# Kernel optimization log

Hardware: AMD Instinct MI355X
Metric: run time of the kernel (lower is better)

Reference implementation:

```python
import jax, jax.numpy as jnp
import numpy as np
from jax import lax

DN = ('NCHW', 'OIHW', 'NCHW')
BN_EPS = 1e-5


def _conv(x, w, pad):
    # pad: list of (lo, hi) for H, W
    return lax.conv_general_dilated(x, w, (1, 1), pad, dimension_numbers=DN)


def _grid_sample_bilinear(img, grid):
    """F.grid_sample(img, grid, align_corners=True, padding_mode='zeros').
    img: [N,C,H,W], grid: [N,Ho,Wo,2] with (x,y) in [-1,1]."""
    N, C, H, W = img.shape
    gx, gy = grid[..., 0], grid[..., 1]
    # align_corners=True mapping to pixel coords
    ix = (gx + 1.0) * 0.5 * (W - 1)
    iy = (gy + 1.0) * 0.5 * (H - 1)
    x0 = jnp.floor(ix)
    y0 = jnp.floor(iy)
    x1 = x0 + 1.0
    y1 = y0 + 1.0
    # bilinear weights
    wa = (x1 - ix) * (y1 - iy)  # top-left (x0,y0)
    wb = (ix - x0) * (y1 - iy)  # top-right (x1,y0)
    wc = (x1 - ix) * (iy - y0)  # bottom-left (x0,y1)
    wd = (ix - x0) * (iy - y0)  # bottom-right (x1,y1)

    imgc = jnp.transpose(img, (0, 2, 3, 1))  # [N,H,W,C]
    b = jnp.arange(N)[:, None, None]

    def gather(xi, yi):
        valid = (xi >= 0) & (xi <= W - 1) & (yi >= 0) & (yi <= H - 1)
        xc = jnp.clip(xi, 0, W - 1).astype(jnp.int32)
        yc = jnp.clip(yi, 0, H - 1).astype(jnp.int32)
        v = imgc[b, yc, xc]  # [N,Ho,Wo,C]
        return v * valid[..., None].astype(img.dtype)

    out = (gather(x0, y0) * wa[..., None] + gather(x1, y0) * wb[..., None]
           + gather(x0, y1) * wc[..., None] + gather(x1, y1) * wd[..., None])
    return jnp.transpose(out, (0, 3, 1, 2))  # [N,C,Ho,Wo]


def setup_inputs() -> dict:
    key = jax.random.key(0)
    ks = jax.random.split(key, 12)
    N, C1, C2 = 8, 512, 256
    H, W = 64, 64
    x1 = jax.random.normal(ks[0], (N, C1, 2 * H, 2 * W), dtype=jnp.float32)
    x2 = jax.random.normal(ks[1], (N, C2, H, W), dtype=jnp.float32)
    w_change = jax.random.normal(ks[2], (C2, C1, 1, 1), dtype=jnp.float32) * 0.02
    b_change = jax.random.normal(ks[3], (C2,), dtype=jnp.float32) * 0.02
    w_cc1 = jax.random.normal(ks[4], (C2, 2 * C2, 1, 1), dtype=jnp.float32) * 0.02
    bn_gamma = 1.0 + 0.1 * jax.random.normal(ks[5], (C2,), dtype=jnp.float32)
    bn_beta = 0.1 * jax.random.normal(ks[6], (C2,), dtype=jnp.float32)
    bn_mean = 0.1 * jax.random.normal(ks[7], (C2,), dtype=jnp.float32)
    bn_var = jax.random.uniform(ks[8], (C2,), dtype=jnp.float32, minval=0.5, maxval=1.5)
    w_cc2 = jax.random.normal(ks[9], (4, C2, 3, 3), dtype=jnp.float32) * 0.02
    return {"x1": x1, "x2": x2, "w_change": w_change, "b_change": b_change,
            "w_cc1": w_cc1, "bn_gamma": bn_gamma, "bn_beta": bn_beta,
            "bn_mean": bn_mean, "bn_var": bn_var, "w_cc2": w_cc2}


def reference(x1, x2, w_change, b_change, w_cc1, bn_gamma, bn_beta, bn_mean, bn_var, w_cc2):
    # MaxPool2d(2,2)
    x1p = lax.reduce_window(x1, -jnp.inf, lax.max, (1, 1, 2, 2), (1, 1, 2, 2), 'VALID')
    # change: 1x1 conv with bias
    x1c = _conv(x1p, w_change, [(0, 0), (0, 0)]) + b_change[None, :, None, None]
    # concat + concat_conv (1x1 conv -> BN(eval) -> ReLU -> 3x3 conv)
    x = jnp.concatenate([x1c, x2], axis=1)
    x = _conv(x, w_cc1, [(0, 0), (0, 0)])
    inv = lax.rsqrt(bn_var + BN_EPS)
    x = (x - bn_mean[None, :, None, None]) * (inv * bn_gamma)[None, :, None, None] + bn_beta[None, :, None, None]
    x = jax.nn.relu(x)
    flow = _conv(x, w_cc2, [(1, 1), (1, 1)])  # [N,4,H,W]
    flow1 = flow[:, :2]
    flow2 = flow[:, 2:]

    N, _, H, W = x1c.shape
    # base grid: [...,0]=x over width, [...,1]=y over height
    xs = jnp.linspace(-1.0, 1.0, W, dtype=x1c.dtype)
    ys = jnp.linspace(-1.0, 1.0, H, dtype=x1c.dtype)
    base = jnp.stack(jnp.meshgrid(xs, ys, indexing='xy'), axis=-1)  # [H,W,2]
    norm = jnp.array([(W - 1) / 2.0, (H - 1) / 2.0], dtype=x1c.dtype)

    grid1 = base[None] + jnp.transpose(flow1, (0, 2, 3, 1)) / norm
    grid2 = base[None] + jnp.transpose(flow2, (0, 2, 3, 1)) / norm

    u1 = _grid_sample_bilinear(x1c, grid1)
    u2 = _grid_sample_bilinear(x2, grid2)
    return u1 + u2
```

## Files before the change

kernel.cpp:

```cpp
#include <hip/hip_runtime.h>
#include <hip/hip_bf16.h>

#define NB 8
#define C1 512
#define C2 256
#define HWSZ 4096
#define BN_EPS 1e-5f
#define P2 264

typedef __hip_bfloat16 bf16;
typedef __hip_bfloat162 bf162;
typedef __attribute__((ext_vector_type(8))) short short8v;
typedef __attribute__((ext_vector_type(4))) float f32x4;

static __device__ inline float us2f(unsigned short u) {
  union { unsigned u32; float f; } c; c.u32 = ((unsigned)u) << 16; return c.f;
}

static __device__ inline unsigned short f2bf(float f) {
  union { bf16 h; unsigned short u; } c;
  c.h = __float2bfloat16(f);
  return c.u;
}

static __device__ inline unsigned pack2(float a, float b) {
  union { unsigned u; bf162 h; } pk;
  pk.h = __float22bfloat162_rn(make_float2(a, b));
  return pk.u;
}

static __device__ inline uint2 pack4(float a, float b, float c, float d) {
  union { uint2 u; bf162 h[2]; } pk;
  pk.h[0] = __float22bfloat162_rn(make_float2(a, b));
  pk.h[1] = __float22bfloat162_rn(make_float2(c, d));
  return pk.u;
}

#define SWA(m_, c_)  (((((c_) >> 3) ^ (((m_) >> 3) & 3)) << 3) + ((c_) & 7))
#define SWA2(m_, c_) (((((c_) >> 3) ^ (((m_) >> 3) & 7)) << 3) + ((c_) & 7))

#define SBARQ() asm volatile("s_waitcnt lgkmcnt(0)\n\ts_barrier" ::: "memory")
#define SBAR()  asm volatile("s_barrier" ::: "memory")
#define LGKM0() asm volatile("s_waitcnt lgkmcnt(0)" ::: "memory")

__global__ __launch_bounds__(256) void k0_prep(
    const float* __restrict__ wch, const float* __restrict__ wcc1,
    const float* __restrict__ wcc2,
    unsigned short* __restrict__ wchB, unsigned short* __restrict__ wcc1B,
    float* __restrict__ wr, float* __restrict__ flow) {
  const int t = blockIdx.x * 256 + threadIdx.x;
  if (t < 262144) {
    const int which = t >> 17;
    const int r = t & 131071;
    const int i = r & 7;
    const int lane = (r >> 3) & 63;
    const int ntile = (r >> 9) & 15;
    const int kstep = r >> 13;
    const int ci = kstep * 32 + (lane >> 4) * 8 + i;
    const int co = ntile * 16 + (lane & 15);
    const float* s = which ? wcc1 : wch;
    unsigned short* d = which ? wcc1B : wchB;
    d[r] = f2bf(s[co * 512 + ci]);
  } else if (t < 262144 + 9216) {
    const int r = t - 262144;
    const int f = r / 2304;
    const int rr = r % 2304;
    const int ci = rr / 9;
    const int tt = rr % 9;
    wr[ci * 36 + (tt / 3) * 12 + (tt % 3) * 4 + f] = wcc2[r];
  } else if (t < 262144 + 9216 + 131072) {
    flow[t - 262144 - 9216] = 0.f;
  }
}

__global__ __launch_bounds__(512) void k12_fused(
    const float* __restrict__ x1, const float* __restrict__ x2,
    const unsigned short* __restrict__ wchB, const unsigned short* __restrict__ wcc1B,
    const float* __restrict__ bch,
    const float* __restrict__ gamma, const float* __restrict__ beta,
    const float* __restrict__ mean, const float* __restrict__ var,
    const float* __restrict__ wr,
    unsigned short* __restrict__ x1c_nhwc, unsigned short* __restrict__ x2_nhwc,
    float* __restrict__ flow) {
  __shared__ unsigned short As[64 * 40];
  __shared__ unsigned short As2[64 * P2];
  const int tid = threadIdx.x;
  const int lane = tid & 63;
  const int wv = tid >> 6;
  const int lrow = lane & 15;
  const int lgrp = lane >> 4;

  const int m0g = blockIdx.x * 64;
  const int n = m0g >> 12;
  const int hw0 = m0g & 4095;
  const int h = hw0 >> 6;

  f32x4 acc[4][2];
#pragma unroll
  for (int mt = 0; mt < 4; ++mt)
#pragma unroll
    for (int nt = 0; nt < 2; ++nt) acc[mt][nt] = (f32x4){0.f, 0.f, 0.f, 0.f};

  const int pmi = tid & 31;
  const int ms = pmi * 2;
  const int ch0 = (tid >> 5) * 2;

  const float* x1p = x1 + (size_t)n * C1 * 16384 + (size_t)(2 * h) * 128 + 2 * ms;

  float4 t0, b0, t1, b1;
#define LOADA(K0_) do { \
    const float* p_ = x1p + (size_t)((K0_) + ch0) * 16384; \
    t0 = *(const float4*)p_;            b0 = *(const float4*)(p_ + 128); \
    t1 = *(const float4*)(p_ + 16384);  b1 = *(const float4*)(p_ + 16384 + 128); \
  } while (0)
#define POOLA(U0_, U1_) do { \
    U0_ = pack2(fmaxf(fmaxf(t0.x, t0.y), fmaxf(b0.x, b0.y)), \
                fmaxf(fmaxf(t1.x, t1.y), fmaxf(b1.x, b1.y))); \
    U1_ = pack2(fmaxf(fmaxf(t0.z, t0.w), fmaxf(b0.z, b0.w)), \
                fmaxf(fmaxf(t1.z, t1.w), fmaxf(b1.z, b1.w))); \
  } while (0)

  unsigned uA0, uA1;
  LOADA(0);
  POOLA(uA0, uA1);
  LOADA(32);

  for (int ks = 0; ks < 16; ++ks) {
    SBARQ();
    *(unsigned*)&As[ms * 40 + SWA(ms, ch0)] = uA0;
    *(unsigned*)&As[(ms + 1) * 40 + SWA(ms + 1, ch0)] = uA1;
    LGKM0();
    SBAR();

    unsigned uN0, uN1;
    if (ks < 15) {
      POOLA(uN0, uN1);
      if (ks < 14) LOADA((ks + 2) * 32);
    }

    short8v a[4];
#pragma unroll
    for (int mt = 0; mt < 4; ++mt) {
      const int m = mt * 16 + lrow;
      a[mt] = *(const short8v*)&As[m * 40 + SWA(m, lgrp * 8)];
    }
#pragma unroll
    for (int nt = 0; nt < 2; ++nt) {
      const int ntile = wv * 2 + nt;
      const short8v b = *(const short8v*)&wchB[(size_t)((ks * 16 + ntile) * 64 + lane) * 8];
#pragma unroll
      for (int mt = 0; mt < 4; ++mt)
        acc[mt][nt] = __builtin_amdgcn_mfma_f32_16x16x32_bf16(a[mt], b, acc[mt][nt], 0, 0, 0);
    }
    if (ks < 15) { uA0 = uN0; uA1 = uN1; }
  }

  const int chB = tid >> 4;
  const int mqB = (tid & 15) * 4;
  float4 cf0 = *(const float4*)&x2[((size_t)(n * C2 + chB)) * HWSZ + hw0 + mqB];
  float4 cf1 = *(const float4*)&x2[((size_t)(n * C2 + 32 + chB)) * HWSZ + hw0 + mqB];

#pragma unroll
  for (int nt = 0; nt < 2; ++nt) {
    const int co = (wv * 2 + nt) * 16 + lrow;
    const float bias = bch[co];
#pragma unroll
    for (int mt = 0; mt < 4; ++mt) {
      const f32x4 v = acc[mt][nt];
      const uint2 pk = pack4(v.x + bias, v.y + bias, v.z + bias, v.w + bias);
      const int mb = mt * 16 + lgrp * 4;
      As2[(mb + 0) * P2 + SWA2(mb + 0, co)] = (unsigned short)(pk.x & 0xffffu);
      As2[(mb + 1) * P2 + SWA2(mb + 1, co)] = (unsigned short)(pk.x >> 16);
      As2[(mb + 2) * P2 + SWA2(mb + 2, co)] = (unsigned short)(pk.y & 0xffffu);
      As2[(mb + 3) * P2 + SWA2(mb + 3, co)] = (unsigned short)(pk.y >> 16);
      acc[mt][nt] = (f32x4){0.f, 0.f, 0.f, 0.f};
    }
  }
  LGKM0();
  SBAR();

  {
    const int mm = tid >> 3;
    const int cg = (tid & 7) * 32;
    const size_t ob = ((size_t)(m0g + mm)) * 256 + cg;
#pragma unroll
    for (int k = 0; k < 4; ++k) {
      const uint4 v = *(const uint4*)&As2[mm * P2 + SWA2(mm, cg + k * 8)];
      *(uint4*)&x1c_nhwc[ob + k * 8] = v;
    }
  }

#pragma unroll
  for (int ks = 0; ks < 8; ++ks) {
    short8v a[4];
#pragma unroll
    for (int mt = 0; mt < 4; ++mt) {
      const int m = mt * 16 + lrow;
      a[mt] = *(const short8v*)&As2[m * P2 + SWA2(m, ks * 32 + lgrp * 8)];
    }
#pragma unroll
    for (int nt = 0; nt < 2; ++nt) {
      const int ntile = wv * 2 + nt;
      const short8v b = *(const short8v*)&wcc1B[(size_t)((ks * 16 + ntile) * 64 + lane) * 8];
#pragma unroll
      for (int mt = 0; mt < 4; ++mt)
        acc[mt][nt] = __builtin_amdgcn_mfma_f32_16x16x32_bf16(a[mt], b, acc[mt][nt], 0, 0, 0);
    }
  }

  for (int ks = 8; ks < 16; ++ks) {
    const unsigned p0 = pack2(cf0.x, cf0.y);
    const unsigned p1 = pack2(cf0.z, cf0.w);
    cf0 = cf1;
    if (ks < 14) {
      cf1 = *(const float4*)&x2[((size_t)(n * C2 + (ks - 6) * 32 + chB)) * HWSZ + hw0 + mqB];
    }
    SBARQ();
    As[(mqB + 0) * 40 + SWA(mqB + 0, chB)] = (unsigned short)(p0 & 0xffffu);
    As[(mqB + 1) * 40 + SWA(mqB + 1, chB)] = (unsigned short)(p0 >> 16);
    As[(mqB + 2) * 40 + SWA(mqB + 2, chB)] = (unsigned short)(p1 & 0xffffu);
    As[(mqB + 3) * 40 + SWA(mqB + 3, chB)] = (unsigned short)(p1 >> 16);
    LGKM0();
    SBAR();

    {
      const int m = tid >> 3;
      const int c4 = (tid & 7) * 4;
      const uint2 v = *(const uint2*)&As[m * 40 + SWA(m, c4)];
      *(uint2*)&x2_nhwc[((size_t)(m0g + m)) * 256 + (ks - 8) * 32 + c4] = v;
    }

    short8v a[4];
#pragma unroll
    for (int mt = 0; mt < 4; ++mt) {
      const int m = mt * 16 + lrow;
      a[mt] = *(const short8v*)&As[m * 40 + SWA(m, lgrp * 8)];
    }
#pragma unroll
    for (int nt = 0; nt < 2; ++nt) {
      const int ntile = wv * 2 + nt;
      const short8v b = *(const short8v*)&wcc1B[(size_t)((ks * 16 + ntile) * 64 + lane) * 8];
#pragma unroll
      for (int mt = 0; mt < 4; ++mt)
        acc[mt][nt] = __builtin_amdgcn_mfma_f32_16x16x32_bf16(a[mt], b, acc[mt][nt], 0, 0, 0);
    }
  }

  SBARQ();
#pragma unroll
  for (int nt = 0; nt < 2; ++nt) {
    const int co = (wv * 2 + nt) * 16 + lrow;
    const float sc = gamma[co] * rsqrtf(var[co] + BN_EPS);
    const float sh = beta[co] - mean[co] * sc;
#pragma unroll
    for (int mt = 0; mt < 4; ++mt) {
      const f32x4 vv = acc[mt][nt];
      const uint2 pk = pack4(fmaxf(vv.x * sc + sh, 0.f), fmaxf(vv.y * sc + sh, 0.f),
                             fmaxf(vv.z * sc + sh, 0.f), fmaxf(vv.w * sc + sh, 0.f));
      const int mb = mt * 16 + lgrp * 4;
      As2[(mb + 0) * P2 + SWA2(mb + 0, co)] = (unsigned short)(pk.x & 0xffffu);
      As2[(mb + 1) * P2 + SWA2(mb + 1, co)] = (unsigned short)(pk.x >> 16);
      As2[(mb + 2) * P2 + SWA2(mb + 2, co)] = (unsigned short)(pk.y & 0xffffu);
      As2[(mb + 3) * P2 + SWA2(mb + 3, co)] = (unsigned short)(pk.y >> 16);
    }
  }
  LGKM0();
  SBAR();

  {
    const int xp = tid & 63;
    const int fh = tid >> 6;
    const int f = fh & 3;
    const int half = fh >> 2;
    float pm = 0.f, pz = 0.f, pp = 0.f;
    for (int ci = half * 128; ci < half * 128 + 128; ci += 2) {
      const float* w0 = wr + ci * 36 + f;
#pragma unroll
      for (int dx = 0; dx < 3; ++dx) {
        const int xs = xp + dx - 1;
        if ((unsigned)xs >= 64u) continue;
        const unsigned vv = *(const unsigned*)&As2[xs * P2 + SWA2(xs, ci)];
        const float v0 = us2f((unsigned short)(vv & 0xffffu));
        const float v1 = us2f((unsigned short)(vv >> 16));
        const float* wa = w0 + dx * 4;
        const float* wb = wa + 36;
        pm = fmaf(v0, wa[24], fmaf(v1, wb[24], pm));
        pz = fmaf(v0, wa[12], fmaf(v1, wb[12], pz));
        pp = fmaf(v0, wa[0],  fmaf(v1, wb[0],  pp));
      }
    }
    float* fb = flow + ((size_t)(n * 4 + f)) * HWSZ + xp;
    if (h >= 1)  atomicAdd(fb + (h - 1) * 64, pm);
    atomicAdd(fb + h * 64, pz);
    if (h <= 62) atomicAdd(fb + (h + 1) * 64, pp);
  }
#undef LOADA
#undef POOLA
}

__global__ __launch_bounds__(1024) void k4_sample(
    const float* __restrict__ flow,
    const unsigned short* __restrict__ x1c_nhwc,
    const unsigned short* __restrict__ x2_nhwc,
    float* __restrict__ out) {
  __shared__ float outT[256][65];
  __shared__ float flr[4][64];
  __shared__ int   toff[8][64];
  __shared__ float twt[8][64];

  const int tid = threadIdx.x;
  const int n = blockIdx.x >> 6;
  const int h = blockIdx.x & 63;
  const int wl = tid & 63;
  const int q = tid >> 6;

  if (tid < 256) {
    flr[tid >> 6][tid & 63] =
        flow[((size_t)(n * 4 + (tid >> 6))) * HWSZ + h * 64 + (tid & 63)];
  }
  __syncthreads();

  if (tid < 64) {
    const float fxv[2] = {flr[0][tid], flr[2][tid]};
    const float fyv[2] = {flr[1][tid], flr[3][tid]};
#pragma unroll
    for (int s = 0; s < 2; ++s) {
      const float ix = (float)tid + fxv[s], iy = (float)h + fyv[s];
      const float x0f = floorf(ix), y0f = floorf(iy);
      const float fx = ix - x0f, fy = iy - y0f;
      const int x0 = (int)x0f, y0 = (int)y0f, x1i = x0 + 1, y1i = y0 + 1;
      const float vx0 = (x0 >= 0 && x0 < 64) ? 1.f : 0.f;
      const float vx1 = (x1i >= 0 && x1i < 64) ? 1.f : 0.f;
      const float vy0 = (y0 >= 0 && y0 < 64) ? 1.f : 0.f;
      const float vy1 = (y1i >= 0 && y1i < 64) ? 1.f : 0.f;
      const int cx0 = min(max(x0, 0), 63), cx1 = min(max(x1i, 0), 63);
      const int cy0 = min(max(y0, 0), 63), cy1 = min(max(y1i, 0), 63);
      toff[s * 4 + 0][tid] = cy0 * 64 + cx0;
      toff[s * 4 + 1][tid] = cy0 * 64 + cx1;
      toff[s * 4 + 2][tid] = cy1 * 64 + cx0;
      toff[s * 4 + 3][tid] = cy1 * 64 + cx1;
      twt[s * 4 + 0][tid] = (1.f - fx) * (1.f - fy) * vx0 * vy0;
      twt[s * 4 + 1][tid] = fx * (1.f - fy) * vx1 * vy0;
      twt[s * 4 + 2][tid] = (1.f - fx) * fy * vx0 * vy1;
      twt[s * 4 + 3][tid] = fx * fy * vx1 * vy1;
    }
  }
  __syncthreads();

  {
    const unsigned short* pb1 = x1c_nhwc + (size_t)n * HWSZ * 256 + wl * 4;
    const unsigned short* pb2 = x2_nhwc + (size_t)n * HWSZ * 256 + wl * 4;
#pragma unroll
    for (int pp = 0; pp < 4; ++pp) {
      const int p = q * 4 + pp;
      float u0 = 0.f, u1 = 0.f, u2 = 0.f, u3 = 0.f;
#pragma unroll
      for (int t = 0; t < 8; ++t) {
        const int off = toff[t][p];
        const float wt = twt[t][p];
        const unsigned short* rp = (t < 4 ? pb1 : pb2) + (size_t)off * 256;
        const uint2 v = *(const uint2*)rp;
        u0 = fmaf(wt, us2f((unsigned short)(v.x & 0xffffu)), u0);
        u1 = fmaf(wt, us2f((unsigned short)(v.x >> 16)), u1);
        u2 = fmaf(wt, us2f((unsigned short)(v.y & 0xffffu)), u2);
        u3 = fmaf(wt, us2f((unsigned short)(v.y >> 16)), u3);
      }
      outT[wl * 4 + 0][p] = u0;
      outT[wl * 4 + 1][p] = u1;
      outT[wl * 4 + 2][p] = u2;
      outT[wl * 4 + 3][p] = u3;
    }
  }
  __syncthreads();

  {
    const int p = tid & 63;
    const int cg = (tid >> 6) * 16;
    const size_t ob = ((size_t)(n * C2 + cg)) * HWSZ + h * 64 + p;
#pragma unroll
    for (int j = 0; j < 16; ++j) {
      out[ob + (size_t)j * HWSZ] = outT[cg + j][p];
    }
  }
}

extern "C" void kernel_launch(void* const* d_in, const int* in_sizes, int n_in,
                              void* d_out, int out_size, void* d_ws, size_t ws_size,
                              hipStream_t stream) {
  const float* x1      = (const float*)d_in[0];
  const float* x2      = (const float*)d_in[1];
  const float* w_change= (const float*)d_in[2];
  const float* b_change= (const float*)d_in[3];
  const float* w_cc1   = (const float*)d_in[4];
  const float* bn_gamma= (const float*)d_in[5];
  const float* bn_beta = (const float*)d_in[6];
  const float* bn_mean = (const float*)d_in[7];
  const float* bn_var  = (const float*)d_in[8];
  const float* w_cc2   = (const float*)d_in[9];
  float* out = (float*)d_out;

  unsigned short* x1c_nhwc = (unsigned short*)d_ws;
  unsigned short* x2_nhwc  = (unsigned short*)((char*)d_ws + (16u << 20));
  float*          flow     = (float*)((char*)d_ws + (32u << 20));
  unsigned short* wchB     = (unsigned short*)((char*)d_ws + (32u << 20) + (512u << 10));
  unsigned short* wcc1B    = (unsigned short*)((char*)d_ws + (32u << 20) + (768u << 10));
  float*          wr       = (float*)((char*)d_ws + (33u << 20));

  k0_prep<<<1572, 256, 0, stream>>>(w_change, w_cc1, w_cc2, wchB, wcc1B, wr, flow);
  k12_fused<<<512, 512, 0, stream>>>(x1, x2, wchB, wcc1B, b_change,
                                     bn_gamma, bn_beta, bn_mean, bn_var, wr,
                                     x1c_nhwc, x2_nhwc, flow);
  k4_sample<<<512, 1024, 0, stream>>>(flow, x1c_nhwc, x2_nhwc, out);
}
```

Baseline: 140.0 us.

## Double fused GEMM block to 1024 threads, one N-tile per wave

The fused pool+1x1conv+concat-conv kernel now launches 1024 threads per block instead of 512. Each of the 16 waves owns a single 16-wide output-channel tile rather than two. Pooling loads, x2 staging, NHWC stores and the 3x3 flow reduction are all re-split across twice as many threads, each doing half the work. This is meant to raise wave-level parallelism and latency hiding per block, at the cost of more barrier participants, narrower per-thread memory accesses, and duplicated A-fragment LDS reads across more waves.

```diff
diff --git a/kernel.cpp b/kernel.cpp
--- a/kernel.cpp
+++ b/kernel.cpp
@@ -21,12 +21,6 @@
   union { bf16 h; unsigned short u; } c;
   c.h = __float2bfloat16(f);
   return c.u;
-}
-
-static __device__ inline unsigned pack2(float a, float b) {
-  union { unsigned u; bf162 h; } pk;
-  pk.h = __float22bfloat162_rn(make_float2(a, b));
-  return pk.u;
 }
 
 static __device__ inline uint2 pack4(float a, float b, float c, float d) {
@@ -73,7 +67,7 @@
   }
 }
 
-__global__ __launch_bounds__(512) void k12_fused(
+__global__ __launch_bounds__(1024) void k12_fused(
     const float* __restrict__ x1, const float* __restrict__ x2,
     const unsigned short* __restrict__ wchB, const unsigned short* __restrict__ wcc1B,
     const float* __restrict__ bch,
@@ -95,47 +89,43 @@
   const int hw0 = m0g & 4095;
   const int h = hw0 >> 6;
 
-  f32x4 acc[4][2];
-#pragma unroll
-  for (int mt = 0; mt < 4; ++mt)
-#pragma unroll
-    for (int nt = 0; nt < 2; ++nt) acc[mt][nt] = (f32x4){0.f, 0.f, 0.f, 0.f};
+  f32x4 acc[4];
+#pragma unroll
+  for (int mt = 0; mt < 4; ++mt) acc[mt] = (f32x4){0.f, 0.f, 0.f, 0.f};
 
   const int pmi = tid & 31;
   const int ms = pmi * 2;
-  const int ch0 = (tid >> 5) * 2;
+  const int chA = tid >> 5;
 
   const float* x1p = x1 + (size_t)n * C1 * 16384 + (size_t)(2 * h) * 128 + 2 * ms;
 
-  float4 t0, b0, t1, b1;
+  float4 t0, b0;
 #define LOADA(K0_) do { \
-    const float* p_ = x1p + (size_t)((K0_) + ch0) * 16384; \
-    t0 = *(const float4*)p_;            b0 = *(const float4*)(p_ + 128); \
-    t1 = *(const float4*)(p_ + 16384);  b1 = *(const float4*)(p_ + 16384 + 128); \
+    const float* p_ = x1p + (size_t)((K0_) + chA) * 16384; \
+    t0 = *(const float4*)p_;  b0 = *(const float4*)(p_ + 128); \
   } while (0)
 #define POOLA(U0_, U1_) do { \
-    U0_ = pack2(fmaxf(fmaxf(t0.x, t0.y), fmaxf(b0.x, b0.y)), \
-                fmaxf(fmaxf(t1.x, t1.y), fmaxf(b1.x, b1.y))); \
-    U1_ = pack2(fmaxf(fmaxf(t0.z, t0.w), fmaxf(b0.z, b0.w)), \
-                fmaxf(fmaxf(t1.z, t1.w), fmaxf(b1.z, b1.w))); \
+    U0_ = f2bf(fmaxf(fmaxf(t0.x, t0.y), fmaxf(b0.x, b0.y))); \
+    U1_ = f2bf(fmaxf(fmaxf(t0.z, t0.w), fmaxf(b0.z, b0.w))); \
   } while (0)
 
-  unsigned uA0, uA1;
+  unsigned short uA0, uA1;
   LOADA(0);
   POOLA(uA0, uA1);
   LOADA(32);
 
   for (int ks = 0; ks < 16; ++ks) {
     SBARQ();
-    *(unsigned*)&As[ms * 40 + SWA(ms, ch0)] = uA0;
-    *(unsigned*)&As[(ms + 1) * 40 + SWA(ms + 1, ch0)] = uA1;
+    As[ms * 40 + SWA(ms, chA)] = uA0;
+    As[(ms + 1) * 40 + SWA(ms + 1, chA)] = uA1;
     LGKM0();
     SBAR();
 
-    unsigned uN0, uN1;
     if (ks < 15) {
+      unsigned short uN0, uN1;
       POOLA(uN0, uN1);
       if (ks < 14) LOADA((ks + 2) * 32);
+      uA0 = uN0; uA1 = uN1;
     }
 
     short8v a[4];
@@ -144,47 +134,41 @@
       const int m = mt * 16 + lrow;
       a[mt] = *(const short8v*)&As[m * 40 + SWA(m, lgrp * 8)];
     }
-#pragma unroll
-    for (int nt = 0; nt < 2; ++nt) {
-      const int ntile = wv * 2 + nt;
-      const short8v b = *(const short8v*)&wchB[(size_t)((ks * 16 + ntile) * 64 + lane) * 8];
-#pragma unroll
-      for (int mt = 0; mt < 4; ++mt)
-        acc[mt][nt] = __builtin_amdgcn_mfma_f32_16x16x32_bf16(a[mt], b, acc[mt][nt], 0, 0, 0);
-    }
-    if (ks < 15) { uA0 = uN0; uA1 = uN1; }
-  }
-
-  const int chB = tid >> 4;
-  const int mqB = (tid & 15) * 4;
-  float4 cf0 = *(const float4*)&x2[((size_t)(n * C2 + chB)) * HWSZ + hw0 + mqB];
-  float4 cf1 = *(const float4*)&x2[((size_t)(n * C2 + 32 + chB)) * HWSZ + hw0 + mqB];
-
-#pragma unroll
-  for (int nt = 0; nt < 2; ++nt) {
-    const int co = (wv * 2 + nt) * 16 + lrow;
+    const short8v b = *(const short8v*)&wchB[(size_t)((ks * 16 + wv) * 64 + lane) * 8];
+#pragma unroll
+    for (int mt = 0; mt < 4; ++mt)
+      acc[mt] = __builtin_amdgcn_mfma_f32_16x16x32_bf16(a[mt], b, acc[mt], 0, 0, 0);
+  }
+
+  const int chB = tid >> 5;
+  const int mqB = (tid & 31) * 2;
+  float2 cf0 = *(const float2*)&x2[((size_t)(n * C2 + chB)) * HWSZ + hw0 + mqB];
+  float2 cf1 = *(const float2*)&x2[((size_t)(n * C2 + 32 + chB)) * HWSZ + hw0 + mqB];
+
+  {
+    const int co = wv * 16 + lrow;
     const float bias = bch[co];
 #pragma unroll
     for (int mt = 0; mt < 4; ++mt) {
-      const f32x4 v = acc[mt][nt];
+      const f32x4 v = acc[mt];
       const uint2 pk = pack4(v.x + bias, v.y + bias, v.z + bias, v.w + bias);
       const int mb = mt * 16 + lgrp * 4;
       As2[(mb + 0) * P2 + SWA2(mb + 0, co)] = (unsigned short)(pk.x & 0xffffu);
       As2[(mb + 1) * P2 + SWA2(mb + 1, co)] = (unsigned short)(pk.x >> 16);
       As2[(mb + 2) * P2 + SWA2(mb + 2, co)] = (unsigned short)(pk.y & 0xffffu);
       As2[(mb + 3) * P2 + SWA2(mb + 3, co)] = (unsigned short)(pk.y >> 16);
-      acc[mt][nt] = (f32x4){0.f, 0.f, 0.f, 0.f};
+      acc[mt] = (f32x4){0.f, 0.f, 0.f, 0.f};
     }
   }
   LGKM0();
   SBAR();
 
   {
-    const int mm = tid >> 3;
-    const int cg = (tid & 7) * 32;
+    const int mm = tid >> 4;
+    const int cg = (tid & 15) * 16;
     const size_t ob = ((size_t)(m0g + mm)) * 256 + cg;
 #pragma unroll
-    for (int k = 0; k < 4; ++k) {
+    for (int k = 0; k < 2; ++k) {
       const uint4 v = *(const uint4*)&As2[mm * P2 + SWA2(mm, cg + k * 8)];
       *(uint4*)&x1c_nhwc[ob + k * 8] = v;
     }
@@ -198,36 +182,30 @@
       const int m = mt * 16 + lrow;
       a[mt] = *(const short8v*)&As2[m * P2 + SWA2(m, ks * 32 + lgrp * 8)];
     }
-#pragma unroll
-    for (int nt = 0; nt < 2; ++nt) {
-      const int ntile = wv * 2 + nt;
-      const short8v b = *(const short8v*)&wcc1B[(size_t)((ks * 16 + ntile) * 64 + lane) * 8];
-#pragma unroll
-      for (int mt = 0; mt < 4; ++mt)
-        acc[mt][nt] = __builtin_amdgcn_mfma_f32_16x16x32_bf16(a[mt], b, acc[mt][nt], 0, 0, 0);
-    }
+    const short8v b = *(const short8v*)&wcc1B[(size_t)((ks * 16 + wv) * 64 + lane) * 8];
+#pragma unroll
+    for (int mt = 0; mt < 4; ++mt)
+      acc[mt] = __builtin_amdgcn_mfma_f32_16x16x32_bf16(a[mt], b, acc[mt], 0, 0, 0);
   }
 
   for (int ks = 8; ks < 16; ++ks) {
-    const unsigned p0 = pack2(cf0.x, cf0.y);
-    const unsigned p1 = pack2(cf0.z, cf0.w);
+    const unsigned short p0 = f2bf(cf0.x);
+    const unsigned short p1 = f2bf(cf0.y);
     cf0 = cf1;
     if (ks < 14) {
-      cf1 = *(const float4*)&x2[((size_t)(n * C2 + (ks - 6) * 32 + chB)) * HWSZ + hw0 + mqB];
+      cf1 = *(const float2*)&x2[((size_t)(n * C2 + (ks - 6) * 32 + chB)) * HWSZ + hw0 + mqB];
     }
     SBARQ();
-    As[(mqB + 0) * 40 + SWA(mqB + 0, chB)] = (unsigned short)(p0 & 0xffffu);
-    As[(mqB + 1) * 40 + SWA(mqB + 1, chB)] = (unsigned short)(p0 >> 16);
-    As[(mqB + 2) * 40 + SWA(mqB + 2, chB)] = (unsigned short)(p1 & 0xffffu);
-    As[(mqB + 3) * 40 + SWA(mqB + 3, chB)] = (unsigned short)(p1 >> 16);
+    As[(mqB + 0) * 40 + SWA(mqB + 0, chB)] = p0;
+    As[(mqB + 1) * 40 + SWA(mqB + 1, chB)] = p1;
     LGKM0();
     SBAR();
 
     {
-      const int m = tid >> 3;
-      const int c4 = (tid & 7) * 4;
-      const uint2 v = *(const uint2*)&As[m * 40 + SWA(m, c4)];
-      *(uint2*)&x2_nhwc[((size_t)(m0g + m)) * 256 + (ks - 8) * 32 + c4] = v;
+      const int m = tid >> 4;
+      const int c2 = (tid & 15) * 2;
+      const unsigned v = *(const unsigned*)&As[m * 40 + SWA(m, c2)];
+      *(unsigned*)&x2_nhwc[((size_t)(m0g + m)) * 256 + (ks - 8) * 32 + c2] = v;
     }
 
     short8v a[4];
@@ -236,25 +214,20 @@
       const int m = mt * 16 + lrow;
       a[mt] = *(const short8v*)&As[m * 40 + SWA(m, lgrp * 8)];
     }
-#pragma unroll
-    for (int nt = 0; nt < 2; ++nt) {
-      const int ntile = wv * 2 + nt;
-      const short8v b = *(const short8v*)&wcc1B[(size_t)((ks * 16 + ntile) * 64 + lane) * 8];
-#pragma unroll
-      for (int mt = 0; mt < 4; ++mt)
-        acc[mt][nt] = __builtin_amdgcn_mfma_f32_16x16x32_bf16(a[mt], b, acc[mt][nt], 0, 0, 0);
-    }
+    const short8v b = *(const short8v*)&wcc1B[(size_t)((ks * 16 + wv) * 64 + lane) * 8];
+#pragma unroll
+    for (int mt = 0; mt < 4; ++mt)
+      acc[mt] = __builtin_amdgcn_mfma_f32_16x16x32_bf16(a[mt], b, acc[mt], 0, 0, 0);
   }
 
   SBARQ();
-#pragma unroll
-  for (int nt = 0; nt < 2; ++nt) {
-    const int co = (wv * 2 + nt) * 16 + lrow;
+  {
+    const int co = wv * 16 + lrow;
     const float sc = gamma[co] * rsqrtf(var[co] + BN_EPS);
     const float sh = beta[co] - mean[co] * sc;
 #pragma unroll
     for (int mt = 0; mt < 4; ++mt) {
-      const f32x4 vv = acc[mt][nt];
+      const f32x4 vv = acc[mt];
       const uint2 pk = pack4(fmaxf(vv.x * sc + sh, 0.f), fmaxf(vv.y * sc + sh, 0.f),
                              fmaxf(vv.z * sc + sh, 0.f), fmaxf(vv.w * sc + sh, 0.f));
       const int mb = mt * 16 + lgrp * 4;
@@ -271,9 +244,9 @@
     const int xp = tid & 63;
     const int fh = tid >> 6;
     const int f = fh & 3;
-    const int half = fh >> 2;
+    const int quarter = fh >> 2;
     float pm = 0.f, pz = 0.f, pp = 0.f;
-    for (int ci = half * 128; ci < half * 128 + 128; ci += 2) {
+    for (int ci = quarter * 64; ci < quarter * 64 + 64; ci += 2) {
       const float* w0 = wr + ci * 36 + f;
 #pragma unroll
       for (int dx = 0; dx < 3; ++dx) {
@@ -407,8 +380,8 @@
   float*          wr       = (float*)((char*)d_ws + (33u << 20));
 
   k0_prep<<<1572, 256, 0, stream>>>(w_change, w_cc1, w_cc2, wchB, wcc1B, wr, flow);
-  k12_fused<<<512, 512, 0, stream>>>(x1, x2, wchB, wcc1B, b_change,
-                                     bn_gamma, bn_beta, bn_mean, bn_var, wr,
-                                     x1c_nhwc, x2_nhwc, flow);
+  k12_fused<<<512, 1024, 0, stream>>>(x1, x2, wchB, wcc1B, b_change,
+                                      bn_gamma, bn_beta, bn_mean, bn_var, wr,
+                                      x1c_nhwc, x2_nhwc, flow);
   k4_sample<<<512, 1024, 0, stream>>>(flow, x1c_nhwc, x2_nhwc, out);
 }
```

Result: faster. 135.0 us, median of 3 (-3.6%).
